# Kernel tuning notes

Hardware: AMD Instinct MI355X
Metric: run time of the kernel (lower is better)

Reference implementation:

```python
import jax, jax.numpy as jnp
import numpy as np

POOL = (7, 7)          # pool_size from init
CROP = (14, 14)        # crop_size = [p*2 for p in pool_size]


def setup_inputs() -> dict:
    key = jax.random.key(0)
    kf, kxy, kwh = jax.random.split(key, 3)
    H_img, W_img = 800, 800
    feature = jax.random.normal(kf, (1, 50, 50, 512), dtype=jnp.float32)
    N = 1024
    # valid boxes: x1<x2, y1<y2, inside the 800x800 image
    xy1 = jax.random.uniform(kxy, (N, 2), minval=0.0, maxval=600.0)
    wh = jax.random.uniform(kwh, (N, 2), minval=32.0, maxval=200.0)
    xy2 = jnp.clip(xy1 + wh, 0.0, 799.0)
    rois = jnp.concatenate([xy1[:, 0:1], xy1[:, 1:2], xy2[:, 0:1], xy2[:, 1:2]], axis=1)  # (x1,y1,x2,y2)
    img_size = jnp.array([H_img, W_img], dtype=jnp.int32)  # (H, W)
    return {"feature": feature, "rois": rois, "img_size": img_size}


def _roi_pool(feature, rois, img_size):
    H, W = feature.shape[1], feature.shape[2]
    ch, cw = CROP
    ih = img_size[0].astype(jnp.float32)
    iw = img_size[1].astype(jnp.float32)
    # normalize rois (x1,y1,x2,y2) by [W,H,W,H], reorder to (y1,x1,y2,x2)
    x1 = rois[:, 0] / iw
    y1 = rois[:, 1] / ih
    x2 = rois[:, 2] / iw
    y2 = rois[:, 3] / ih
    # TF crop_and_resize sampling grid (crop size > 1 branch)
    gy = jnp.arange(ch, dtype=jnp.float32)
    gx = jnp.arange(cw, dtype=jnp.float32)
    in_y = y1[:, None] * (H - 1) + gy[None, :] * ((y2 - y1) * (H - 1) / (ch - 1))[:, None]  # [N,ch]
    in_x = x1[:, None] * (W - 1) + gx[None, :] * ((x2 - x1) * (W - 1) / (cw - 1))[:, None]  # [N,cw]
    top = jnp.floor(in_y)
    left = jnp.floor(in_x)
    ly = in_y - top   # [N,ch]
    lx = in_x - left  # [N,cw]
    t = jnp.clip(top, 0, H - 1).astype(jnp.int32)
    b = jnp.clip(top + 1, 0, H - 1).astype(jnp.int32)
    l = jnp.clip(left, 0, W - 1).astype(jnp.int32)
    r = jnp.clip(left + 1, 0, W - 1).astype(jnp.int32)
    img = feature[0]  # box_ind is all zeros -> single image [H,W,C]
    tl = img[t[:, :, None], l[:, None, :]]  # [N,ch,cw,C]
    tr = img[t[:, :, None], r[:, None, :]]
    bl = img[b[:, :, None], l[:, None, :]]
    br = img[b[:, :, None], r[:, None, :]]
    lyE = ly[:, :, None, None]
    lxE = lx[:, None, :, None]
    crops = (tl * (1 - lyE) * (1 - lxE) + tr * (1 - lyE) * lxE
             + bl * lyE * (1 - lxE) + br * lyE * lxE)
    # extrapolation_value = 0 outside [0, dim-1]
    valid = (((in_y >= 0) & (in_y <= H - 1))[:, :, None]
             & ((in_x >= 0) & (in_x <= W - 1))[:, None, :])
    crops = jnp.where(valid[..., None], crops, 0.0)
    # 2x2 max pool, stride 2 (crop dims are even so SAME == VALID)
    N, C = crops.shape[0], crops.shape[-1]
    pooled = crops.reshape(N, ch // 2, 2, cw // 2, 2, C).max(axis=(2, 4))  # [N,7,7,C]
    return pooled


def reference(feature, rois, img_size):
    return _roi_pool(feature, rois, img_size)
```

## Files before the change

### kernel.cpp

```cpp
#include <hip/hip_runtime.h>

#define FH 50
#define FW 50
#define FC 512
#define NROI 1024
#define ROWBYTES (FW * FC * 4)
#define COLBYTES (FC * 4)

typedef float f4v __attribute__((ext_vector_type(4)));

__device__ __forceinline__ float uflane(float v) {
    return __int_as_float(__builtin_amdgcn_readfirstlane(__float_as_int(v)));
}

__device__ __forceinline__ float4 lerp4(float4 a, float4 b, float t) {
    float4 r;
    r.x = fmaf(t, b.x - a.x, a.x);
    r.y = fmaf(t, b.y - a.y, a.y);
    r.z = fmaf(t, b.z - a.z, a.z);
    r.w = fmaf(t, b.w - a.w, a.w);
    return r;
}

__device__ __forceinline__ float4 max44(float4 a, float4 b) {
    float4 r;
    r.x = fmaxf(a.x, b.x);
    r.y = fmaxf(a.y, b.y);
    r.z = fmaxf(a.z, b.z);
    r.w = fmaxf(a.w, b.w);
    return r;
}

__global__ __launch_bounds__(256, 6) void roi_pool_kernel(
    const float* __restrict__ feature,
    const float* __restrict__ rois,
    const int*   __restrict__ img_size,
    float*       __restrict__ out)
{
    int tid  = threadIdx.x;
    int wid  = (blockIdx.x * 256 + tid) >> 6;
    wid = __builtin_amdgcn_readfirstlane(wid);
    int lane = tid & 63;

    int n    = wid / 14;
    int rem  = wid - n * 14;
    int py   = rem >> 1;
    int half = rem & 1;

    float ih = (float)__builtin_amdgcn_readfirstlane(img_size[0]);
    float iw = (float)__builtin_amdgcn_readfirstlane(img_size[1]);
    const float* rp = rois + (size_t)n * 4;
    float x1 = uflane(rp[0]) / iw;
    float y1 = uflane(rp[1]) / ih;
    float x2 = uflane(rp[2]) / iw;
    float y2 = uflane(rp[3]) / ih;

    const float HM1 = 49.0f;
    float sy = (y2 - y1) * HM1 / 13.0f;
    float sx = (x2 - x1) * HM1 / 13.0f;
    float oy = y1 * HM1;
    float ox = x1 * HM1;

    float iy0 = oy + (float)(2 * py)     * sy;
    float iy1 = oy + (float)(2 * py + 1) * sy;
    float fy0 = floorf(iy0), fy1 = floorf(iy1);
    float ly0 = iy0 - fy0,   ly1 = iy1 - fy1;
    int t0 = __builtin_amdgcn_readfirstlane((int)fy0);
    int t1 = __builtin_amdgcn_readfirstlane((int)fy1);
    int adv = t1 - t0;

    const char* rA = (const char*)feature + (size_t)half * 1024
                   + (size_t)t0 * ROWBYTES;

    int curL = __builtin_amdgcn_readfirstlane((int)floorf(ox));
    int voff = curL * COLBYTES + lane * 16;

    auto loadcol = [&](int vo, float4& V0, float4& V1) {
        float4 A = *reinterpret_cast<const float4*>(rA + vo);
        float4 B = *reinterpret_cast<const float4*>(rA + ROWBYTES + vo);
        V0 = lerp4(A, B, ly0);
        if (adv) {
            float4 D = *reinterpret_cast<const float4*>(rA + 2 * ROWBYTES + vo);
            V1 = lerp4(B, D, ly1);
        } else {
            V1 = lerp4(A, B, ly1);
        }
    };

    float4 VA0, VA1, VB0, VB1;
    loadcol(voff,            VA0, VA1);
    loadcol(voff + COLBYTES, VB0, VB1);
    int voffN = voff + 2 * COLBYTES;

    float* obase = out + ((size_t)n * 49 + (size_t)py * 7) * FC + half * 256 + lane * 4;

    float4 m;
#pragma unroll 2
    for (int j = 0; j < 14; ++j) {
        float ix = ox + (float)j * sx;
        float fx = floorf(ix);
        int   lj = (int)fx;
        float lx = ix - fx;
        while (lj > curL) {
            ++curL;
            VA0 = VB0; VA1 = VB1;
            loadcol(voffN, VB0, VB1);
            voffN += COLBYTES;
        }
        float4 s0 = lerp4(VA0, VB0, lx);
        float4 s1 = lerp4(VA1, VB1, lx);
        float4 sm = max44(s0, s1);
        if (j & 1) {
            m = max44(m, sm);
            __builtin_nontemporal_store(*reinterpret_cast<f4v*>(&m),
                reinterpret_cast<f4v*>(obase + (size_t)(j >> 1) * FC));
        } else {
            m = sm;
        }
    }
}

extern "C" void kernel_launch(void* const* d_in, const int* in_sizes, int n_in,
                              void* d_out, int out_size, void* d_ws, size_t ws_size,
                              hipStream_t stream) {
    const float* feature  = (const float*)d_in[0];
    const float* rois     = (const float*)d_in[1];
    const int*   img_size = (const int*)d_in[2];
    float* out = (float*)d_out;

    int blocks = NROI * 14 / 4;
    roi_pool_kernel<<<blocks, 256, 0, stream>>>(feature, rois, img_size, out);
}
```

Before: 32.12 us.

## Software-pipeline column loads two slots ahead in ROI pool kernel

Restructures the inner column loop so feature-column loads are issued two columns ahead into double-buffered registers, with consumption of output samples driven by the column index. The goal is to hide global-memory load latency that the previous just-in-time load inside the while loop exposed. The output stores also change from nontemporal to plain stores. In exchange it needs more live registers, which at launch bounds of 256 threads with 6 blocks may cause spilling or lower occupancy. The control flow is also more complex, and the column-to-sample matching relies on float floor consistency.

```diff
diff --git a/kernel.cpp b/kernel.cpp
--- a/kernel.cpp
+++ b/kernel.cpp
@@ -72,52 +72,73 @@
     const char* rA = (const char*)feature + (size_t)half * 1024
                    + (size_t)t0 * ROWBYTES;
 
-    int curL = __builtin_amdgcn_readfirstlane((int)floorf(ox));
-    int voff = curL * COLBYTES + lane * 16;
+    int c0u   = __builtin_amdgcn_readfirstlane((int)floorf(ox));
+    int lumax = __builtin_amdgcn_readfirstlane((int)floorf(ox + 13.0f * sx));
+    int ncols = lumax + 2 - c0u;
 
-    auto loadcol = [&](int vo, float4& V0, float4& V1) {
-        float4 A = *reinterpret_cast<const float4*>(rA + vo);
-        float4 B = *reinterpret_cast<const float4*>(rA + ROWBYTES + vo);
-        V0 = lerp4(A, B, ly0);
-        if (adv) {
-            float4 D = *reinterpret_cast<const float4*>(rA + 2 * ROWBYTES + vo);
-            V1 = lerp4(B, D, ly1);
-        } else {
-            V1 = lerp4(A, B, ly1);
-        }
-    };
+    int lane16 = lane * 16;
 
-    float4 VA0, VA1, VB0, VB1;
-    loadcol(voff,            VA0, VA1);
-    loadcol(voff + COLBYTES, VB0, VB1);
-    int voffN = voff + 2 * COLBYTES;
+#define ISSUE(slot, A, B, D)                                                    \
+    {                                                                           \
+        int vo = (c0u + (slot)) * COLBYTES + lane16;                            \
+        A = *reinterpret_cast<const float4*>(rA + vo);                          \
+        B = *reinterpret_cast<const float4*>(rA + ROWBYTES + vo);               \
+        if (adv) {                                                              \
+            D = *reinterpret_cast<const float4*>(rA + 2 * ROWBYTES + vo);       \
+        }                                                                       \
+    }
+
+    float4 p0A, p0B, p0D;
+    float4 p1A, p1B, p1D;
+    ISSUE(0, p0A, p0B, p0D);
+    ISSUE(1, p1A, p1B, p1D);
 
     float* obase = out + ((size_t)n * 49 + (size_t)py * 7) * FC + half * 256 + lane * 4;
 
-    float4 m;
-#pragma unroll 2
-    for (int j = 0; j < 14; ++j) {
-        float ix = ox + (float)j * sx;
-        float fx = floorf(ix);
-        int   lj = (int)fx;
-        float lx = ix - fx;
-        while (lj > curL) {
-            ++curL;
-            VA0 = VB0; VA1 = VB1;
-            loadcol(voffN, VB0, VB1);
-            voffN += COLBYTES;
+    float4 Vp0, Vp1;
+    float4 m = make_float4(0.f, 0.f, 0.f, 0.f);
+    int j = 0;
+
+#define CONSUME(scol)                                                           \
+    while (j < 14) {                                                            \
+        float ix = ox + (float)j * sx;                                          \
+        float fx = floorf(ix);                                                  \
+        if ((int)fx != (scol) + c0u - 1) break;                                 \
+        float lx = ix - fx;                                                     \
+        float4 s0 = lerp4(Vp0, Vc0, lx);                                        \
+        float4 s1 = lerp4(Vp1, Vc1, lx);                                        \
+        float4 sm = max44(s0, s1);                                              \
+        if (j & 1) {                                                            \
+            m = max44(m, sm);                                                   \
+            *reinterpret_cast<f4v*>(obase + (size_t)(j >> 1) * FC) =            \
+                *reinterpret_cast<f4v*>(&m);                                    \
+        } else {                                                                \
+            m = sm;                                                             \
+        }                                                                       \
+        ++j;                                                                    \
+    }
+
+    for (int s = 0; s < ncols; s += 2) {
+        {
+            float4 rAe = p0A, rBe = p0B, rDe = p0D;
+            if (s + 2 < ncols) ISSUE(s + 2, p0A, p0B, p0D);
+            float4 Vc0 = lerp4(rAe, rBe, ly0);
+            float4 Vc1 = adv ? lerp4(rBe, rDe, ly1) : lerp4(rAe, rBe, ly1);
+            if (s >= 1) { CONSUME(s); }
+            Vp0 = Vc0; Vp1 = Vc1;
         }
-        float4 s0 = lerp4(VA0, VB0, lx);
-        float4 s1 = lerp4(VA1, VB1, lx);
-        float4 sm = max44(s0, s1);
-        if (j & 1) {
-            m = max44(m, sm);
-            __builtin_nontemporal_store(*reinterpret_cast<f4v*>(&m),
-                reinterpret_cast<f4v*>(obase + (size_t)(j >> 1) * FC));
-        } else {
-            m = sm;
+        if (s + 1 < ncols) {
+            float4 rAo = p1A, rBo = p1B, rDo = p1D;
+            if (s + 3 < ncols) ISSUE(s + 3, p1A, p1B, p1D);
+            float4 Vc0 = lerp4(rAo, rBo, ly0);
+            float4 Vc1 = adv ? lerp4(rBo, rDo, ly1) : lerp4(rAo, rBo, ly1);
+            CONSUME(s + 1);
+            Vp0 = Vc0; Vp1 = Vc1;
         }
     }
+
+#undef ISSUE
+#undef CONSUME
 }
 
 extern "C" void kernel_launch(void* const* d_in, const int* in_sizes, int n_in,
```

Result: slower. 36.59 us (+13.9%).
